# Optimization experiments

Measured on AMD Instinct MI355X. Metric: run time of the kernel, lower is better.

## Reference

```python
import jax, jax.numpy as jnp
import numpy as np

B, S, D, R = 64, 1024, 768, 4


def setup_inputs() -> dict:
    key = jax.random.key(0)
    ks = jax.random.split(key, 8)
    x = jax.random.normal(ks[0], (B, S, D), dtype=jnp.float32)
    W_qkv = jax.random.normal(ks[1], (3 * D, D), dtype=jnp.float32) * 0.02
    b_qkv = jax.random.normal(ks[2], (3 * D,), dtype=jnp.float32) * 0.02
    A_q = jax.random.normal(ks[3], (R, D), dtype=jnp.float32) * 0.02
    B_q = jax.random.normal(ks[4], (D, R), dtype=jnp.float32) * 0.02
    A_v = jax.random.normal(ks[5], (R, D), dtype=jnp.float32) * 0.02
    B_v = jax.random.normal(ks[6], (D, R), dtype=jnp.float32) * 0.02
    s0 = jax.random.uniform(ks[7], (1,), dtype=jnp.float32)
    return {"x": x, "W_qkv": W_qkv, "b_qkv": b_qkv,
            "A_q": A_q, "B_q": B_q, "A_v": A_v, "B_v": B_v, "s0": s0}


def reference(x, W_qkv, b_qkv, A_q, B_q, A_v, B_v, s0):
    # Base qkv projection: [B, S, 3D]
    qkv = jnp.einsum('bsd,ed->bse', x, W_qkv) + b_qkv
    # Source code overwrites the per-task loop accumulation with the last
    # task's LoRA delta scaled by scaling_factor[0] (no norm division),
    # so the effective output adds only that delta.
    new_q = s0[0] * jnp.einsum('bsr,dr->bsd', jnp.einsum('bsd,rd->bsr', x, A_q), B_q)
    new_v = s0[0] * jnp.einsum('bsr,dr->bsd', jnp.einsum('bsd,rd->bsr', x, A_v), B_v)
    qkv = qkv.at[:, :, :D].add(new_q)
    qkv = qkv.at[:, :, 2 * D:].add(new_v)
    return qkv
```

## Files before the change

### kernel.cpp

```cpp
#include <hip/hip_runtime.h>
#include <stdint.h>

#define D_DIM   768
#define N_DIM   2304
#define M_DIM   65536
#define BM      128
#define BN      128
#define BK      32

typedef short v8ss __attribute__((ext_vector_type(8)));
typedef float v4f  __attribute__((ext_vector_type(4)));

__device__ __forceinline__ unsigned short f2bf(float f) {
    union { float f; uint32_t u; } v; v.f = f;
    uint32_t r = v.u + 0x7fffu + ((v.u >> 16) & 1u);
    return (unsigned short)(r >> 16);
}

__global__ void prep_w(const float* __restrict__ W,
                       const float* __restrict__ Aq, const float* __restrict__ Bq,
                       const float* __restrict__ Av, const float* __restrict__ Bv,
                       const float* __restrict__ s0,
                       unsigned short* __restrict__ Weff) {
    int idx = blockIdx.x * 256 + threadIdx.x;
    int e = idx / D_DIM;
    int k = idx - e * D_DIM;
    float w = W[idx];
    float s = s0[0];
    if (e < D_DIM) {
        float acc = 0.f;
#pragma unroll
        for (int r = 0; r < 4; r++) acc += Bq[e * 4 + r] * Aq[r * D_DIM + k];
        w += s * acc;
    } else if (e >= 2 * D_DIM) {
        int d = e - 2 * D_DIM;
        float acc = 0.f;
#pragma unroll
        for (int r = 0; r < 4; r++) acc += Bv[d * 4 + r] * Av[r * D_DIM + k];
        w += s * acc;
    }
    Weff[idx] = f2bf(w);
}

__global__ void convert_x(const float* __restrict__ x,
                          unsigned short* __restrict__ xb, int n4) {
    int stride = gridDim.x * blockDim.x;
    for (int i = blockIdx.x * blockDim.x + threadIdx.x; i < n4; i += stride) {
        float4 v = ((const float4*)x)[i];
        ushort4 o;
        o.x = f2bf(v.x); o.y = f2bf(v.y); o.z = f2bf(v.z); o.w = f2bf(v.w);
        ((ushort4*)xb)[i] = o;
    }
}

template <bool XB16>
__global__ __launch_bounds__(256, 2) void gemm_bt(const void* __restrict__ Aptr,
                                                  const unsigned short* __restrict__ Weff,
                                                  const float* __restrict__ bias,
                                                  float* __restrict__ out) {
    __shared__ __align__(16) unsigned short As[BM * BK];
    __shared__ __align__(16) unsigned short Bs[BN * BK];

    const int tid = threadIdx.x;
    const int l   = tid & 63;
    const int w   = tid >> 6;
    const int wm  = w & 1;
    const int wn  = w >> 1;
    const int n0  = blockIdx.x * BN;
    const int m0  = blockIdx.y * BM;

    v4f acc[4][4];
#pragma unroll
    for (int i = 0; i < 4; i++)
#pragma unroll
        for (int j = 0; j < 4; j++) acc[i][j] = (v4f){0.f, 0.f, 0.f, 0.f};

    const int lq  = l >> 4;
    const int l15 = l & 15;

    for (int k0 = 0; k0 < D_DIM; k0 += BK) {
        __syncthreads();

        if (XB16) {
            const unsigned short* xb = (const unsigned short*)Aptr;
#pragma unroll
            for (int c = 0; c < 2; c++) {
                int mloc = c * 64 + w * 16 + (l >> 2);
                int kloc = (l & 3) * 8;
                const unsigned short* g = xb + (size_t)(m0 + mloc) * D_DIM + k0 + kloc;
                __builtin_amdgcn_global_load_lds(
                    (const __attribute__((address_space(1))) void*)g,
                    (__attribute__((address_space(3))) void*)(As + c * 2048 + w * 512),
                    16, 0, 0);
            }
        } else {
            const float* x = (const float*)Aptr;
#pragma unroll
            for (int p = 0; p < 4; p++) {
                int row = p * 32 + (tid >> 3);
                int kk  = (tid & 7) * 4;
                float4 v = *(const float4*)(x + (size_t)(m0 + row) * D_DIM + k0 + kk);
                ushort4 o;
                o.x = f2bf(v.x); o.y = f2bf(v.y); o.z = f2bf(v.z); o.w = f2bf(v.w);
                *(ushort4*)&As[row * BK + kk] = o;
            }
        }

#pragma unroll
        for (int c = 0; c < 2; c++) {
            int nloc = c * 64 + w * 16 + (l >> 2);
            int kloc = (l & 3) * 8;
            const unsigned short* g = Weff + (size_t)(n0 + nloc) * D_DIM + k0 + kloc;
            __builtin_amdgcn_global_load_lds(
                (const __attribute__((address_space(1))) void*)g,
                (__attribute__((address_space(3))) void*)(Bs + c * 2048 + w * 512),
                16, 0, 0);
        }

        __syncthreads();

        v8ss a_frag[4], b_frag[4];
#pragma unroll
        for (int mt = 0; mt < 4; mt++)
            a_frag[mt] = *(const v8ss*)&As[(wm * 64 + mt * 16 + l15) * BK + lq * 8];
#pragma unroll
        for (int nt = 0; nt < 4; nt++)
            b_frag[nt] = *(const v8ss*)&Bs[(wn * 64 + nt * 16 + l15) * BK + lq * 8];

#pragma unroll
        for (int mt = 0; mt < 4; mt++)
#pragma unroll
            for (int nt = 0; nt < 4; nt++)
                acc[mt][nt] = __builtin_amdgcn_mfma_f32_16x16x32_bf16(
                    a_frag[mt], b_frag[nt], acc[mt][nt], 0, 0, 0);
    }

#pragma unroll
    for (int nt = 0; nt < 4; nt++) {
        int col = n0 + wn * 64 + nt * 16 + l15;
        float bv = bias[col];
#pragma unroll
        for (int mt = 0; mt < 4; mt++) {
            int row = m0 + wm * 64 + mt * 16 + lq * 4;
            float* o = out + (size_t)row * N_DIM + col;
#pragma unroll
            for (int i = 0; i < 4; i++)
                o[(size_t)i * N_DIM] = acc[mt][nt][i] + bv;
        }
    }
}

extern "C" void kernel_launch(void* const* d_in, const int* in_sizes, int n_in,
                              void* d_out, int out_size, void* d_ws, size_t ws_size,
                              hipStream_t stream) {
    const float* x   = (const float*)d_in[0];
    const float* W   = (const float*)d_in[1];
    const float* b   = (const float*)d_in[2];
    const float* Aq  = (const float*)d_in[3];
    const float* Bq  = (const float*)d_in[4];
    const float* Av  = (const float*)d_in[5];
    const float* Bv  = (const float*)d_in[6];
    const float* s0  = (const float*)d_in[7];
    float* out = (float*)d_out;

    unsigned short* Weff = (unsigned short*)d_ws;
    const size_t weff_elems = (size_t)N_DIM * D_DIM;
    const size_t x_elems    = (size_t)M_DIM * D_DIM;
    const size_t need       = weff_elems * 2 + x_elems * 2;

    prep_w<<<(int)(weff_elems / 256), 256, 0, stream>>>(W, Aq, Bq, Av, Bv, s0, Weff);

    dim3 grid(N_DIM / BN, M_DIM / BM);
    if (ws_size >= need) {
        unsigned short* xb = Weff + weff_elems;
        convert_x<<<4096, 256, 0, stream>>>(x, xb, (int)(x_elems / 4));
        gemm_bt<true><<<grid, 256, 0, stream>>>(xb, Weff, b, out);
    } else {
        gemm_bt<false><<<grid, 256, 0, stream>>>(x, Weff, b, out);
    }
}
```

Measured before the change: 1.039 ms.

## Double K-tile with XOR-swizzled LDS, XCD-aware block remap, nontemporal loads/stores

Raises the K tile of the bf16 GEMM from 32 to 64 and stores the A and B tiles in LDS with an XOR swizzle on 16-byte chunks, so fragment reads avoid bank conflicts and each barrier pair covers more MFMA work. The grid becomes 1D, and block ids are remapped so that consecutive tiles land on the same XCD for better L2 reuse. It also uses nontemporal loads in the conversion kernel and nontemporal stores for the large fp32 output, and raises launch_bounds occupancy to 4. The risks are register pressure under the tighter launch bound and LDS doubling to 32KB per block.

Result: faster. 861.6 us (-17.0%).

```diff
diff --git a/kernel.cpp b/kernel.cpp
--- a/kernel.cpp
+++ b/kernel.cpp
@@ -6,7 +6,11 @@
 #define M_DIM   65536
 #define BM      128
 #define BN      128
-#define BK      32
+#define BK      64
+#define NT_X    18
+#define MT_Y    512
+#define NWG     (NT_X * MT_Y)
+#define PER_XCD (NWG / 8)
 
 typedef short v8ss __attribute__((ext_vector_type(8)));
 typedef float v4f  __attribute__((ext_vector_type(4)));
@@ -46,7 +50,7 @@
                           unsigned short* __restrict__ xb, int n4) {
     int stride = gridDim.x * blockDim.x;
     for (int i = blockIdx.x * blockDim.x + threadIdx.x; i < n4; i += stride) {
-        float4 v = ((const float4*)x)[i];
+        v4f v = __builtin_nontemporal_load(((const v4f*)x) + i);
         ushort4 o;
         o.x = f2bf(v.x); o.y = f2bf(v.y); o.z = f2bf(v.z); o.w = f2bf(v.w);
         ((ushort4*)xb)[i] = o;
@@ -54,7 +58,7 @@
 }
 
 template <bool XB16>
-__global__ __launch_bounds__(256, 2) void gemm_bt(const void* __restrict__ Aptr,
+__global__ __launch_bounds__(256, 4) void gemm_bt(const void* __restrict__ Aptr,
                                                   const unsigned short* __restrict__ Weff,
                                                   const float* __restrict__ bias,
                                                   float* __restrict__ out) {
@@ -66,8 +70,13 @@
     const int w   = tid >> 6;
     const int wm  = w & 1;
     const int wn  = w >> 1;
-    const int n0  = blockIdx.x * BN;
-    const int m0  = blockIdx.y * BM;
+
+    const int bid = blockIdx.x;
+    const int swz = (bid & 7) * PER_XCD + (bid >> 3);
+    const int by  = swz / NT_X;
+    const int bx  = swz - by * NT_X;
+    const int n0  = bx * BN;
+    const int m0  = by * BM;
 
     v4f acc[4][4];
 #pragma unroll
@@ -78,16 +87,18 @@
     const int lq  = l >> 4;
     const int l15 = l & 15;
 
+    const int srow = w * 8 + (l >> 3);
+    const int sch  = (l & 7) ^ (l >> 3);
+
     for (int k0 = 0; k0 < D_DIM; k0 += BK) {
         __syncthreads();
 
         if (XB16) {
             const unsigned short* xb = (const unsigned short*)Aptr;
 #pragma unroll
-            for (int c = 0; c < 2; c++) {
-                int mloc = c * 64 + w * 16 + (l >> 2);
-                int kloc = (l & 3) * 8;
-                const unsigned short* g = xb + (size_t)(m0 + mloc) * D_DIM + k0 + kloc;
+            for (int c = 0; c < 4; c++) {
+                const unsigned short* g =
+                    xb + (size_t)(m0 + c * 32 + srow) * D_DIM + k0 + sch * 8;
                 __builtin_amdgcn_global_load_lds(
                     (const __attribute__((address_space(1))) void*)g,
                     (__attribute__((address_space(3))) void*)(As + c * 2048 + w * 512),
@@ -95,22 +106,28 @@
             }
         } else {
             const float* x = (const float*)Aptr;
-#pragma unroll
-            for (int p = 0; p < 4; p++) {
-                int row = p * 32 + (tid >> 3);
-                int kk  = (tid & 7) * 4;
-                float4 v = *(const float4*)(x + (size_t)(m0 + row) * D_DIM + k0 + kk);
-                ushort4 o;
-                o.x = f2bf(v.x); o.y = f2bf(v.y); o.z = f2bf(v.z); o.w = f2bf(v.w);
-                *(ushort4*)&As[row * BK + kk] = o;
-            }
-        }
-
-#pragma unroll
-        for (int c = 0; c < 2; c++) {
-            int nloc = c * 64 + w * 16 + (l >> 2);
-            int kloc = (l & 3) * 8;
-            const unsigned short* g = Weff + (size_t)(n0 + nloc) * D_DIM + k0 + kloc;
+            const int r = tid >> 1;
+            const int h = tid & 1;
+            const float* src = x + (size_t)(m0 + r) * D_DIM + k0 + h * 32;
+#pragma unroll
+            for (int j = 0; j < 4; j++) {
+                float4 v0 = *(const float4*)(src + j * 8);
+                float4 v1 = *(const float4*)(src + j * 8 + 4);
+                int ch = h * 4 + j;
+                int p  = ch ^ (r & 7);
+                v8ss o;
+                o[0] = (short)f2bf(v0.x); o[1] = (short)f2bf(v0.y);
+                o[2] = (short)f2bf(v0.z); o[3] = (short)f2bf(v0.w);
+                o[4] = (short)f2bf(v1.x); o[5] = (short)f2bf(v1.y);
+                o[6] = (short)f2bf(v1.z); o[7] = (short)f2bf(v1.w);
+                *(v8ss*)&As[r * 64 + p * 8] = o;
+            }
+        }
+
+#pragma unroll
+        for (int c = 0; c < 4; c++) {
+            const unsigned short* g =
+                Weff + (size_t)(n0 + c * 32 + srow) * D_DIM + k0 + sch * 8;
             __builtin_amdgcn_global_load_lds(
                 (const __attribute__((address_space(1))) void*)g,
                 (__attribute__((address_space(3))) void*)(Bs + c * 2048 + w * 512),
@@ -119,20 +136,28 @@
 
         __syncthreads();
 
-        v8ss a_frag[4], b_frag[4];
-#pragma unroll
-        for (int mt = 0; mt < 4; mt++)
-            a_frag[mt] = *(const v8ss*)&As[(wm * 64 + mt * 16 + l15) * BK + lq * 8];
-#pragma unroll
-        for (int nt = 0; nt < 4; nt++)
-            b_frag[nt] = *(const v8ss*)&Bs[(wn * 64 + nt * 16 + l15) * BK + lq * 8];
-
-#pragma unroll
-        for (int mt = 0; mt < 4; mt++)
-#pragma unroll
-            for (int nt = 0; nt < 4; nt++)
-                acc[mt][nt] = __builtin_amdgcn_mfma_f32_16x16x32_bf16(
-                    a_frag[mt], b_frag[nt], acc[mt][nt], 0, 0, 0);
+#pragma unroll
+        for (int ks = 0; ks < 2; ks++) {
+            v8ss af[4], bf[4];
+#pragma unroll
+            for (int mt = 0; mt < 4; mt++) {
+                int r = wm * 64 + mt * 16 + l15;
+                int p = (ks * 4 + lq) ^ (l15 & 7);
+                af[mt] = *(const v8ss*)&As[r * 64 + p * 8];
+            }
+#pragma unroll
+            for (int nt = 0; nt < 4; nt++) {
+                int r = wn * 64 + nt * 16 + l15;
+                int p = (ks * 4 + lq) ^ (l15 & 7);
+                bf[nt] = *(const v8ss*)&Bs[r * 64 + p * 8];
+            }
+#pragma unroll
+            for (int mt = 0; mt < 4; mt++)
+#pragma unroll
+                for (int nt = 0; nt < 4; nt++)
+                    acc[mt][nt] = __builtin_amdgcn_mfma_f32_16x16x32_bf16(
+                        af[mt], bf[nt], acc[mt][nt], 0, 0, 0);
+        }
     }
 
 #pragma unroll
@@ -145,7 +170,8 @@
             float* o = out + (size_t)row * N_DIM + col;
 #pragma unroll
             for (int i = 0; i < 4; i++)
-                o[(size_t)i * N_DIM] = acc[mt][nt][i] + bv;
+                __builtin_nontemporal_store(acc[mt][nt][i] + bv,
+                                            o + (size_t)i * N_DIM);
         }
     }
 }
@@ -170,12 +196,11 @@
 
     prep_w<<<(int)(weff_elems / 256), 256, 0, stream>>>(W, Aq, Bq, Av, Bv, s0, Weff);
 
-    dim3 grid(N_DIM / BN, M_DIM / BM);
     if (ws_size >= need) {
         unsigned short* xb = Weff + weff_elems;
         convert_x<<<4096, 256, 0, stream>>>(x, xb, (int)(x_elems / 4));
-        gemm_bt<true><<<grid, 256, 0, stream>>>(xb, Weff, b, out);
+        gemm_bt<true><<<NWG, 256, 0, stream>>>(xb, Weff, b, out);
     } else {
-        gemm_bt<false><<<grid, 256, 0, stream>>>(x, Weff, b, out);
-    }
-}
+        gemm_bt<false><<<NWG, 256, 0, stream>>>(x, Weff, b, out);
+    }
+}
```
